# Performance work log

Measured on AMD Instinct MI355X. Metric: run time of the kernel, lower is better.

The kernel has to match this reference:

```python
import jax, jax.numpy as jnp
import numpy as np

B, S, D, L = 64, 512, 256, 3
NUM_BUCKETS = 1500  # RelativePositionBias default


def _ln(x, g, b):
    m = x.mean(-1, keepdims=True)
    v = x.var(-1, keepdims=True)
    return (x - m) * jax.lax.rsqrt(v + 1e-5) * g + b


def setup_inputs() -> dict:
    key = jax.random.key(0)
    ks = jax.random.split(key, 10)
    s = 0.02
    f32 = jnp.float32
    return dict(
        x=jax.random.normal(ks[0], (B, S, D), f32),
        mask=jnp.ones((B, S), jnp.int32),
        bias_table=jax.random.normal(ks[1], (NUM_BUCKETS,), f32) * s,  # n_heads=1
        ln_g=jnp.ones((L, D), f32), ln_b=jnp.zeros((L, D), f32),
        wq=jax.random.normal(ks[2], (L, D, D), f32) * s, bq=jnp.zeros((L, D), f32),
        wk=jax.random.normal(ks[3], (L, D, D), f32) * s, bk=jnp.zeros((L, D), f32),
        wv=jax.random.normal(ks[4], (L, D, D), f32) * s, bv=jnp.zeros((L, D), f32),
        wo=jax.random.normal(ks[5], (L, D, D), f32) * s, bo=jnp.zeros((L, D), f32),
        cm_ln_g=jnp.ones((L, D), f32), cm_ln_b=jnp.zeros((L, D), f32),
        w1=jax.random.normal(ks[6], (L, D, D), f32) * s, b1=jnp.zeros((L, D), f32),
        w2=jax.random.normal(ks[7], (L, D, D), f32) * s, b2=jnp.zeros((L, D), f32),
    )


def reference(x, mask, bias_table, ln_g, ln_b, wq, bq, wk, bk, wv, bv, wo, bo,
              cm_ln_g, cm_ln_b, w1, b1, w2, b2):
    slen = x.shape[1]
    # relative position bias (RelativePositionBias.compute_bias), n_heads=1
    pos = jnp.arange(slen)
    rel = pos[None, :] - pos[:, None]        # memory - context
    maxn = slen - 1                          # torch.max(rel)
    bucket = jnp.where(rel < 0, -rel + maxn, rel)
    cp = bias_table[bucket]                  # [S, S], broadcasts over batch
    scale = jnp.sqrt(jnp.asarray(x.shape[-1], x.dtype))  # sqrt(hid_dim // 1)
    pad = (mask == 0)[:, None, :]            # [B, 1, S] key-side padding mask
    neg = jnp.finfo(x.dtype).min
    for j in range(L):
        h = _ln(x, ln_g[j], ln_b[j])
        q = h @ wq[j] + bq[j]
        k = h @ wk[j] + bk[j]
        v = h @ wv[j] + bv[j]
        e = jnp.einsum('bqd,bkd->bqk', q, k) / scale + cp
        e = jnp.where(pad, neg, e)
        a = jax.nn.softmax(e, axis=-1)
        o = jnp.einsum('bqk,bkd->bqd', a, v) @ wo[j] + bo[j]
        x = h + _ln(o, ln_g[j], ln_b[j])     # same LayerNorm reused, per source
        c = _ln(x, cm_ln_g[j], cm_ln_b[j])
        x = x + (jax.nn.gelu(c @ w1[j] + b1[j], approximate=False) @ w2[j] + b2[j])
    return x
```

## Files before the change

kernel.cpp:

```cpp
#include <hip/hip_runtime.h>
#include <hip/hip_bf16.h>
#include <math.h>

#define D_HID 256
#define N_B   64
#define S_LEN 512
#define N_L   3
#define M_ROWS (N_B * S_LEN)

typedef __bf16 bf16_t;
typedef __bf16 bf16x8 __attribute__((ext_vector_type(8)));
typedef __bf16 bf16x4 __attribute__((ext_vector_type(4)));
typedef float  f32x4  __attribute__((ext_vector_type(4)));
typedef unsigned int u32;

__device__ __forceinline__ f32x4 mfma16(bf16x8 a, bf16x8 b, f32x4 c) {
    return __builtin_amdgcn_mfma_f32_16x16x32_bf16(a, b, c, 0, 0, 0);
}

__device__ __forceinline__ void gld_lds16(const void* g, void* l) {
    __builtin_amdgcn_global_load_lds((const __attribute__((address_space(1))) u32*)g,
                                     (__attribute__((address_space(3))) u32*)l, 16, 0, 0);
}

__device__ __forceinline__ u32 pk_bf16(float a, float b) {
    return (u32)(__hip_bfloat16_raw(__hip_bfloat16(a)).x) |
           ((u32)(__hip_bfloat16_raw(__hip_bfloat16(b)).x) << 16);
}

__global__ __launch_bounds__(256) void transpose_w(const float* __restrict__ w,
                                                   bf16_t* __restrict__ wt,
                                                   int layer_stride) {
    int i = blockIdx.x * 256 + threadIdx.x;
    int k = i & 255;
    int n = (i >> 8) & 255;
    int l = i >> 16;
    wt[(size_t)l * layer_stride + n * 256 + k] =
        (bf16_t)w[((size_t)l << 16) + ((size_t)k << 8) + n];
}

__global__ __launch_bounds__(256) void ln_fwd(const float* __restrict__ in,
                                              const float* __restrict__ g,
                                              const float* __restrict__ b,
                                              float* __restrict__ H,
                                              bf16_t* __restrict__ Hb) {
    int row  = blockIdx.x * 4 + (threadIdx.x >> 6);
    int lane = threadIdx.x & 63;
    float4 x = ((const float4*)(in + (size_t)row * D_HID))[lane];
    float s  = x.x + x.y + x.z + x.w;
    float sq = x.x * x.x + x.y * x.y + x.z * x.z + x.w * x.w;
#pragma unroll
    for (int o = 1; o < 64; o <<= 1) { s += __shfl_xor(s, o); sq += __shfl_xor(sq, o); }
    float mean = s * (1.f / D_HID);
    float rstd = rsqrtf(sq * (1.f / D_HID) - mean * mean + 1e-5f);
    float4 gv = ((const float4*)g)[lane];
    float4 bv = ((const float4*)b)[lane];
    float4 h;
    h.x = (x.x - mean) * rstd * gv.x + bv.x;
    h.y = (x.y - mean) * rstd * gv.y + bv.y;
    h.z = (x.z - mean) * rstd * gv.z + bv.z;
    h.w = (x.w - mean) * rstd * gv.w + bv.w;
    ((float4*)(H + (size_t)row * D_HID))[lane] = h;
    bf16x4 hb = { (bf16_t)h.x, (bf16_t)h.y, (bf16_t)h.z, (bf16_t)h.w };
    *((bf16x4*)(Hb + (size_t)row * D_HID) + lane) = hb;
}

__global__ __launch_bounds__(256) void ln_res_ln(const float* __restrict__ T,
                                                 const float* __restrict__ H,
                                                 const float* __restrict__ g,
                                                 const float* __restrict__ b,
                                                 const float* __restrict__ cg,
                                                 const float* __restrict__ cb,
                                                 float* __restrict__ X,
                                                 bf16_t* __restrict__ Cb) {
    int row  = blockIdx.x * 4 + (threadIdx.x >> 6);
    int lane = threadIdx.x & 63;
    float4 t = ((const float4*)(T + (size_t)row * D_HID))[lane];
    float s  = t.x + t.y + t.z + t.w;
    float sq = t.x * t.x + t.y * t.y + t.z * t.z + t.w * t.w;
#pragma unroll
    for (int o = 1; o < 64; o <<= 1) { s += __shfl_xor(s, o); sq += __shfl_xor(sq, o); }
    float mean = s * (1.f / D_HID);
    float rstd = rsqrtf(sq * (1.f / D_HID) - mean * mean + 1e-5f);
    float4 gv = ((const float4*)g)[lane];
    float4 bv = ((const float4*)b)[lane];
    float4 hh = ((const float4*)(H + (size_t)row * D_HID))[lane];
    float4 x;
    x.x = hh.x + (t.x - mean) * rstd * gv.x + bv.x;
    x.y = hh.y + (t.y - mean) * rstd * gv.y + bv.y;
    x.z = hh.z + (t.z - mean) * rstd * gv.z + bv.z;
    x.w = hh.w + (t.w - mean) * rstd * gv.w + bv.w;
    ((float4*)(X + (size_t)row * D_HID))[lane] = x;
    float s2  = x.x + x.y + x.z + x.w;
    float sq2 = x.x * x.x + x.y * x.y + x.z * x.z + x.w * x.w;
#pragma unroll
    for (int o = 1; o < 64; o <<= 1) { s2 += __shfl_xor(s2, o); sq2 += __shfl_xor(sq2, o); }
    float mean2 = s2 * (1.f / D_HID);
    float rstd2 = rsqrtf(sq2 * (1.f / D_HID) - mean2 * mean2 + 1e-5f);
    float4 cgv = ((const float4*)cg)[lane];
    float4 cbv = ((const float4*)cb)[lane];
    bf16x4 c = { (bf16_t)((x.x - mean2) * rstd2 * cgv.x + cbv.x),
                 (bf16_t)((x.y - mean2) * rstd2 * cgv.y + cbv.y),
                 (bf16_t)((x.z - mean2) * rstd2 * cgv.z + cbv.z),
                 (bf16_t)((x.w - mean2) * rstd2 * cgv.w + cbv.w) };
    *((bf16x4*)(Cb + (size_t)row * D_HID) + lane) = c;
}

__device__ __forceinline__ void gemm_core(const bf16_t* __restrict__ A,
                                          const bf16_t* __restrict__ W,
                                          int m0, int n0,
                                          bf16_t* As, bf16_t* Bs,
                                          f32x4 (&acc)[4][4]) {
    const int tid  = threadIdx.x;
    const int lane = tid & 63;
    const int wid  = tid >> 6;
    const int wm = wid >> 1, wn = wid & 1;
    const int r = lane & 15, g = lane >> 4;
#pragma unroll 1
    for (int kt = 0; kt < 4; ++kt) {
        if (kt) __syncthreads();
#pragma unroll
        for (int i = 0; i < 4; ++i) {
            const int base8 = i * 256 + wid * 64;
            const int idx8  = base8 + lane;
            const int row   = idx8 >> 3;
            const int sc8   = (idx8 & 7) ^ (row & 7);
            gld_lds16(A + (size_t)(m0 + row) * D_HID + kt * 64 + sc8 * 8, As + base8 * 8);
            gld_lds16(W + (size_t)(n0 + row) * D_HID + kt * 64 + sc8 * 8, Bs + base8 * 8);
        }
        __syncthreads();
#pragma unroll
        for (int ks = 0; ks < 2; ++ks) {
            bf16x8 af[4], bfr[4];
#pragma unroll
            for (int mt = 0; mt < 4; ++mt) {
                const int row = wm * 64 + mt * 16 + r;
                const int c8  = (ks * 4 + g) ^ (row & 7);
                af[mt] = *(const bf16x8*)(As + row * 64 + c8 * 8);
            }
#pragma unroll
            for (int nt = 0; nt < 4; ++nt) {
                const int row = wn * 64 + nt * 16 + r;
                const int c8  = (ks * 4 + g) ^ (row & 7);
                bfr[nt] = *(const bf16x8*)(Bs + row * 64 + c8 * 8);
            }
#pragma unroll
            for (int mt = 0; mt < 4; ++mt)
#pragma unroll
                for (int nt = 0; nt < 4; ++nt)
                    acc[mt][nt] = mfma16(af[mt], bfr[nt], acc[mt][nt]);
        }
    }
}

__global__ __launch_bounds__(256) void gemm_qkv(const bf16_t* __restrict__ A,
                                                const bf16_t* __restrict__ Wp,
                                                const float* __restrict__ bq,
                                                const float* __restrict__ bk,
                                                const float* __restrict__ bv,
                                                bf16_t* __restrict__ Qb,
                                                bf16_t* __restrict__ Kb,
                                                bf16_t* __restrict__ Vt) {
    __shared__ bf16_t As[128 * 64], Bs[128 * 64];
    f32x4 acc[4][4] = {};
    const int m0 = blockIdx.x * 128, n0 = blockIdx.y * 128;
    gemm_core(A, Wp, m0, n0, As, Bs, acc);
    const int lane = threadIdx.x & 63, wid = threadIdx.x >> 6;
    const int wm = wid >> 1, wn = wid & 1, r = lane & 15, g = lane >> 4;
#pragma unroll
    for (int nt = 0; nt < 4; ++nt) {
        const int col = n0 + wn * 64 + nt * 16 + r;
        const int t = col >> 8, cc = col & 255;
        const float bias = (t == 0 ? bq : t == 1 ? bk : bv)[cc];
#pragma unroll
        for (int mt = 0; mt < 4; ++mt)
#pragma unroll
            for (int rr = 0; rr < 4; ++rr) {
                const int row = m0 + wm * 64 + mt * 16 + g * 4 + rr;
                const float v = acc[mt][nt][rr] + bias;
                if (t == 0)      Qb[(size_t)row * D_HID + cc] = (bf16_t)v;
                else if (t == 1) Kb[(size_t)row * D_HID + cc] = (bf16_t)v;
                else             Vt[((size_t)(row >> 9) * D_HID + cc) * S_LEN + (row & 511)] = (bf16_t)v;
            }
    }
}

template <int EPI>
__global__ __launch_bounds__(256) void gemm_one(const bf16_t* __restrict__ A,
                                                const bf16_t* __restrict__ W,
                                                const float* __restrict__ bias,
                                                void* __restrict__ outp,
                                                const float* __restrict__ addsrc) {
    __shared__ bf16_t As[128 * 64], Bs[128 * 64];
    f32x4 acc[4][4] = {};
    const int m0 = blockIdx.x * 128, n0 = blockIdx.y * 128;
    gemm_core(A, W, m0, n0, As, Bs, acc);
    const int lane = threadIdx.x & 63, wid = threadIdx.x >> 6;
    const int wm = wid >> 1, wn = wid & 1, r = lane & 15, g = lane >> 4;
#pragma unroll
    for (int nt = 0; nt < 4; ++nt) {
        const int col = n0 + wn * 64 + nt * 16 + r;
        const float bv = bias[col];
#pragma unroll
        for (int mt = 0; mt < 4; ++mt)
#pragma unroll
            for (int rr = 0; rr < 4; ++rr) {
                const size_t idx = (size_t)(m0 + wm * 64 + mt * 16 + g * 4 + rr) * D_HID + col;
                float v = acc[mt][nt][rr] + bv;
                if constexpr (EPI == 1) {
                    v = 0.5f * v * (1.f + erff(v * 0.70710678118654752f));
                    ((bf16_t*)outp)[idx] = (bf16_t)v;
                } else if constexpr (EPI == 2) {
                    ((float*)outp)[idx] = v;
                } else {
                    ((float*)outp)[idx] = addsrc[idx] + v;
                }
            }
    }
}

__global__ __launch_bounds__(256) void attn_fwd(const bf16_t* __restrict__ Q,
                                                const bf16_t* __restrict__ K,
                                                const bf16_t* __restrict__ Vt,
                                                const float* __restrict__ btab,
                                                const int* __restrict__ mask,
                                                bf16_t* __restrict__ AO) {
    __shared__ float  bias_lds[1024];
    __shared__ float  mask_add[512];
    __shared__ bf16_t P_lds[32 * 64];
    __shared__ float  m_part[4][32], l_part[4][32];
    __shared__ bf16_t o_lds[32][264];

    const int tid = threadIdx.x, lane = tid & 63, w = tid >> 6;
    const int r = lane & 15, g = lane >> 4;

    const int lid = blockIdx.x;
    const int xcd = lid & 7, slot = lid >> 3;
    const int b  = xcd * 8 + (slot >> 4);
    const int q0 = (slot & 15) * 32;

    for (int i = tid; i < 1024; i += 256) {
        const int rel = i - 512;
        const int bucket = (rel < 0) ? (511 - rel) : rel;
        bias_lds[i] = btab[bucket];
    }
    for (int i = tid; i < 512; i += 256)
        mask_add[i] = mask[b * S_LEN + i] ? 0.f : -3.0e38f;
    __syncthreads();

    const bf16_t* Qp = Q  + ((size_t)b * S_LEN + q0) * D_HID;
    const bf16_t* Kp = K  + (size_t)b * S_LEN * D_HID;
    const bf16_t* Vp = Vt + (size_t)b * D_HID * S_LEN;

    f32x4 oacc[4][2] = {};
    float m_run[2] = {-3.0e38f, -3.0e38f};
    float l_run[2] = {0.f, 0.f};

#pragma unroll 1
    for (int kt = 0; kt < 8; ++kt) {
        const int k0 = kt * 64;
        f32x4 sacc[2] = {};
#pragma unroll
        for (int ks = 0; ks < 8; ++ks) {
            const int dk = ks * 32 + g * 8;
            bf16x8 kf  = *(const bf16x8*)(Kp + (size_t)(k0 + w * 16 + r) * D_HID + dk);
            bf16x8 qf0 = *(const bf16x8*)(Qp + (size_t)r * D_HID + dk);
            bf16x8 qf1 = *(const bf16x8*)(Qp + (size_t)(16 + r) * D_HID + dk);
            sacc[0] = mfma16(kf, qf0, sacc[0]);
            sacc[1] = mfma16(kf, qf1, sacc[1]);
        }
        float mx[2] = {-3.0e38f, -3.0e38f};
#pragma unroll
        for (int qb = 0; qb < 2; ++qb) {
            const int qg = q0 + qb * 16 + r;
#pragma unroll
            for (int rr = 0; rr < 4; ++rr) {
                const int kg = k0 + w * 16 + g * 4 + rr;
                float ev = sacc[qb][rr] * 0.0625f + bias_lds[kg - qg + 512] + mask_add[kg];
                sacc[qb][rr] = ev;
                mx[qb] = fmaxf(mx[qb], ev);
            }
            mx[qb] = fmaxf(mx[qb], __shfl_xor(mx[qb], 16));
            mx[qb] = fmaxf(mx[qb], __shfl_xor(mx[qb], 32));
        }
        if (g == 0) { m_part[w][r] = mx[0]; m_part[w][16 + r] = mx[1]; }
        __syncthreads();
        float mnew[2], fac[2];
#pragma unroll
        for (int qb = 0; qb < 2; ++qb) {
            const int q = qb * 16 + r;
            const float tm = fmaxf(fmaxf(m_part[0][q], m_part[1][q]),
                                   fmaxf(m_part[2][q], m_part[3][q]));
            mnew[qb] = fmaxf(m_run[qb], tm);
            fac[qb]  = __expf(m_run[qb] - mnew[qb]);
            m_run[qb] = mnew[qb];
        }
#pragma unroll
        for (int qb = 0; qb < 2; ++qb) {
            const float p0 = __expf(sacc[qb][0] - mnew[qb]);
            const float p1 = __expf(sacc[qb][1] - mnew[qb]);
            const float p2 = __expf(sacc[qb][2] - mnew[qb]);
            const float p3 = __expf(sacc[qb][3] - mnew[qb]);
            float ls = p0 + p1 + p2 + p3;
            ls += __shfl_xor(ls, 16);
            ls += __shfl_xor(ls, 32);
            if (g == 0) l_part[w][qb * 16 + r] = ls;
            const int q = qb * 16 + r;
            const int u = (2 * w + (g >> 1)) ^ (q & 7);
            uint2 pv; pv.x = pk_bf16(p0, p1); pv.y = pk_bf16(p2, p3);
            *(uint2*)((char*)P_lds + q * 128 + u * 16 + (g & 1) * 8) = pv;
        }
        __syncthreads();
#pragma unroll
        for (int qb = 0; qb < 2; ++qb) {
            const int q = qb * 16 + r;
            const float lt = l_part[0][q] + l_part[1][q] + l_part[2][q] + l_part[3][q];
            l_run[qb] = l_run[qb] * fac[qb] + lt;
        }
#pragma unroll
        for (int nt = 0; nt < 4; ++nt)
#pragma unroll
            for (int qb = 0; qb < 2; ++qb)
#pragma unroll
                for (int rr = 0; rr < 4; ++rr)
                    oacc[nt][qb][rr] *= fac[qb];
#pragma unroll
        for (int ks = 0; ks < 2; ++ks) {
            bf16x8 pf[2];
#pragma unroll
            for (int qb = 0; qb < 2; ++qb) {
                const int q = qb * 16 + r;
                const int u = (ks * 4 + g) ^ (q & 7);
                pf[qb] = *(const bf16x8*)((const char*)P_lds + q * 128 + u * 16);
            }
            __builtin_amdgcn_s_setprio(1);
#pragma unroll
            for (int nt = 0; nt < 4; ++nt) {
                bf16x8 vf = *(const bf16x8*)(Vp + (size_t)(w * 64 + nt * 16 + r) * S_LEN
                                                  + k0 + ks * 32 + g * 8);
                oacc[nt][0] = mfma16(vf, pf[0], oacc[nt][0]);
                oacc[nt][1] = mfma16(vf, pf[1], oacc[nt][1]);
            }
            __builtin_amdgcn_s_setprio(0);
        }
    }
    const float inv_l[2] = { 1.f / fmaxf(l_run[0], 1e-30f),
                             1.f / fmaxf(l_run[1], 1e-30f) };
#pragma unroll
    for (int nt = 0; nt < 4; ++nt)
#pragma unroll
        for (int qb = 0; qb < 2; ++qb) {
            const int q = qb * 16 + r;
            const int d = w * 64 + nt * 16 + g * 4;
            bf16x4 ob = { (bf16_t)(oacc[nt][qb][0] * inv_l[qb]),
                          (bf16_t)(oacc[nt][qb][1] * inv_l[qb]),
                          (bf16_t)(oacc[nt][qb][2] * inv_l[qb]),
                          (bf16_t)(oacc[nt][qb][3] * inv_l[qb]) };
            *(bf16x4*)&o_lds[q][d] = ob;
        }
    __syncthreads();
    bf16_t* Op = AO + ((size_t)b * S_LEN + q0) * D_HID;
#pragma unroll
    for (int it = 0; it < 4; ++it) {
        const int idx = it * 256 + tid;
        const int row = idx >> 5, u = idx & 31;
        bf16x8 vv = *(const bf16x8*)&o_lds[row][u * 8];
        *(bf16x8*)(Op + (size_t)row * D_HID + u * 8) = vv;
    }
}

extern "C" void kernel_launch(void* const* d_in, const int* in_sizes, int n_in,
                              void* d_out, int out_size, void* d_ws, size_t ws_size,
                              hipStream_t stream) {
    const float* x_in = (const float*)d_in[0];
    const int*   mask = (const int*)d_in[1];
    const float* btab = (const float*)d_in[2];
    const float* ln_g = (const float*)d_in[3];
    const float* ln_b = (const float*)d_in[4];
    const float* wq = (const float*)d_in[5];
    const float* bq = (const float*)d_in[6];
    const float* wk = (const float*)d_in[7];
    const float* bk = (const float*)d_in[8];
    const float* wv = (const float*)d_in[9];
    const float* bv = (const float*)d_in[10];
    const float* wo = (const float*)d_in[11];
    const float* bo = (const float*)d_in[12];
    const float* cg = (const float*)d_in[13];
    const float* cb = (const float*)d_in[14];
    const float* w1 = (const float*)d_in[15];
    const float* b1 = (const float*)d_in[16];
    const float* w2 = (const float*)d_in[17];
    const float* b2 = (const float*)d_in[18];
    float* out = (float*)d_out;

    char* p = (char*)d_ws;
    const size_t F32SZ  = (size_t)M_ROWS * D_HID * sizeof(float);
    const size_t BF16SZ = (size_t)M_ROWS * D_HID * sizeof(bf16_t);
    float*  H  = (float*)p;  p += F32SZ;
    float*  X  = (float*)p;  p += F32SZ;
    bf16_t* Hb = (bf16_t*)p; p += BF16SZ;
    bf16_t* Qb = (bf16_t*)p; p += BF16SZ;
    bf16_t* Kb = (bf16_t*)p;
    float*  T  = (float*)Kb;
    bf16_t* T1b = Kb;
    p += BF16SZ;
    bf16_t* Vt = (bf16_t*)p; p += BF16SZ;
    bf16_t* Wqkv = (bf16_t*)p; p += (size_t)N_L * 768 * 256 * sizeof(bf16_t);
    bf16_t* Wrest = (bf16_t*)p;
    bf16_t* AO = Hb;
    bf16_t* Cb = Qb;

    const int WELEMS = N_L * D_HID * D_HID;
    transpose_w<<<dim3(WELEMS / 256), dim3(256), 0, stream>>>(wq, Wqkv + 0 * 65536, 3 * 65536);
    transpose_w<<<dim3(WELEMS / 256), dim3(256), 0, stream>>>(wk, Wqkv + 1 * 65536, 3 * 65536);
    transpose_w<<<dim3(WELEMS / 256), dim3(256), 0, stream>>>(wv, Wqkv + 2 * 65536, 3 * 65536);
    transpose_w<<<dim3(WELEMS / 256), dim3(256), 0, stream>>>(wo, Wrest + (size_t)0 * WELEMS, 65536);
    transpose_w<<<dim3(WELEMS / 256), dim3(256), 0, stream>>>(w1, Wrest + (size_t)1 * WELEMS, 65536);
    transpose_w<<<dim3(WELEMS / 256), dim3(256), 0, stream>>>(w2, Wrest + (size_t)2 * WELEMS, 65536);

    const dim3 gblk(256, 1, 1);
    const dim3 grid_qkv(M_ROWS / 128, 6, 1);
    const dim3 grid_one(M_ROWS / 128, 2, 1);

    for (int j = 0; j < N_L; ++j) {
        const bf16_t* WQKVj = Wqkv + (size_t)j * 3 * 65536;
        const bf16_t* WOt = Wrest + ((size_t)0 * N_L + j) * 65536;
        const bf16_t* W1t = Wrest + ((size_t)1 * N_L + j) * 65536;
        const bf16_t* W2t = Wrest + ((size_t)2 * N_L + j) * 65536;

        ln_fwd<<<dim3(M_ROWS / 4), gblk, 0, stream>>>(j == 0 ? x_in : X,
                                                      ln_g + j * D_HID, ln_b + j * D_HID, H, Hb);
        gemm_qkv<<<grid_qkv, gblk, 0, stream>>>(Hb, WQKVj, bq + j * D_HID, bk + j * D_HID,
                                                bv + j * D_HID, Qb, Kb, Vt);
        attn_fwd<<<dim3(N_B * 16, 1, 1), gblk, 0, stream>>>(Qb, Kb, Vt, btab, mask, AO);
        gemm_one<2><<<grid_one, gblk, 0, stream>>>(AO, WOt, bo + j * D_HID, T, nullptr);
        ln_res_ln<<<dim3(M_ROWS / 4), gblk, 0, stream>>>(T, H, ln_g + j * D_HID, ln_b + j * D_HID,
                                                         cg + j * D_HID, cb + j * D_HID, X, Cb);
        gemm_one<1><<<grid_one, gblk, 0, stream>>>(Cb, W1t, b1 + j * D_HID, T1b, nullptr);
        gemm_one<3><<<grid_one, gblk, 0, stream>>>(T1b, W2t, b2 + j * D_HID,
                                                   (j == N_L - 1) ? (void*)out : (void*)X, X);
    }
}
```

Before: 715.8 us.

## Double-buffer GEMM LDS tiles, hoist Q and V loads in attention, fuse transposes

The GEMM core now double-buffers its A/B tiles in LDS, so the next K-tile is fetched while MFMAs run on the current one, and the number of barriers drops. In attention, Q fragments are loaded once into registers and V fragments are prefetched at the start of each key tile, and launch bounds request two blocks per CU. The six weight-transpose launches are merged into one. The cost is twice the GEMM LDS footprint and more registers in attention, which may lower occupancy.

```diff
diff --git a/kernel.cpp b/kernel.cpp
--- a/kernel.cpp
+++ b/kernel.cpp
@@ -28,15 +28,24 @@
            ((u32)(__hip_bfloat16_raw(__hip_bfloat16(b)).x) << 16);
 }
 
-__global__ __launch_bounds__(256) void transpose_w(const float* __restrict__ w,
-                                                   bf16_t* __restrict__ wt,
-                                                   int layer_stride) {
-    int i = blockIdx.x * 256 + threadIdx.x;
-    int k = i & 255;
-    int n = (i >> 8) & 255;
-    int l = i >> 16;
-    wt[(size_t)l * layer_stride + n * 256 + k] =
-        (bf16_t)w[((size_t)l << 16) + ((size_t)k << 8) + n];
+__global__ __launch_bounds__(256) void transpose_all(const float* __restrict__ wq,
+                                                     const float* __restrict__ wk,
+                                                     const float* __restrict__ wv,
+                                                     const float* __restrict__ wo,
+                                                     const float* __restrict__ w1,
+                                                     const float* __restrict__ w2,
+                                                     bf16_t* __restrict__ Wqkv,
+                                                     bf16_t* __restrict__ Wrest) {
+    const int t = blockIdx.y;
+    const float* src = t == 0 ? wq : t == 1 ? wk : t == 2 ? wv
+                     : t == 3 ? wo : t == 4 ? w1 : w2;
+    const int i = blockIdx.x * 256 + threadIdx.x;
+    const int k = i & 255;
+    const int n = (i >> 8) & 255;
+    const int l = i >> 16;
+    const bf16_t v = (bf16_t)src[((size_t)l << 16) + ((size_t)k << 8) + n];
+    if (t < 3) Wqkv[(size_t)l * 3 * 65536 + t * 65536 + n * 256 + k] = v;
+    else       Wrest[(size_t)(t - 3) * 196608 + l * 65536 + n * 256 + k] = v;
 }
 
 __global__ __launch_bounds__(256) void ln_fwd(const float* __restrict__ in,
@@ -106,49 +115,68 @@
     *((bf16x4*)(Cb + (size_t)row * D_HID) + lane) = c;
 }
 
+__device__ __forceinline__ void stage_tile(const bf16_t* __restrict__ A,
+                                           const bf16_t* __restrict__ W,
+                                           int m0, int n0, int kt,
+                                           bf16_t* As, bf16_t* Bs) {
+    const int lane = threadIdx.x & 63;
+    const int wid  = threadIdx.x >> 6;
+#pragma unroll
+    for (int i = 0; i < 4; ++i) {
+        const int base8 = i * 256 + wid * 64;
+        const int idx8  = base8 + lane;
+        const int row   = idx8 >> 3;
+        const int sc8   = (idx8 & 7) ^ (row & 7);
+        gld_lds16(A + (size_t)(m0 + row) * D_HID + kt * 64 + sc8 * 8, As + base8 * 8);
+        gld_lds16(W + (size_t)(n0 + row) * D_HID + kt * 64 + sc8 * 8, Bs + base8 * 8);
+    }
+}
+
+__device__ __forceinline__ void compute_tile(const bf16_t* As, const bf16_t* Bs,
+                                             f32x4 (&acc)[4][4]) {
+    const int lane = threadIdx.x & 63;
+    const int wid  = threadIdx.x >> 6;
+    const int wm = wid >> 1, wn = wid & 1;
+    const int r = lane & 15, g = lane >> 4;
+#pragma unroll
+    for (int ks = 0; ks < 2; ++ks) {
+        bf16x8 af[4], bfr[4];
+#pragma unroll
+        for (int mt = 0; mt < 4; ++mt) {
+            const int row = wm * 64 + mt * 16 + r;
+            const int c8  = (ks * 4 + g) ^ (row & 7);
+            af[mt] = *(const bf16x8*)(As + row * 64 + c8 * 8);
+        }
+#pragma unroll
+        for (int nt = 0; nt < 4; ++nt) {
+            const int row = wn * 64 + nt * 16 + r;
+            const int c8  = (ks * 4 + g) ^ (row & 7);
+            bfr[nt] = *(const bf16x8*)(Bs + row * 64 + c8 * 8);
+        }
+#pragma unroll
+        for (int mt = 0; mt < 4; ++mt)
+#pragma unroll
+            for (int nt = 0; nt < 4; ++nt)
+                acc[mt][nt] = mfma16(af[mt], bfr[nt], acc[mt][nt]);
+    }
+}
+
 __device__ __forceinline__ void gemm_core(const bf16_t* __restrict__ A,
                                           const bf16_t* __restrict__ W,
                                           int m0, int n0,
-                                          bf16_t* As, bf16_t* Bs,
+                                          bf16_t (&As)[2][8192], bf16_t (&Bs)[2][8192],
                                           f32x4 (&acc)[4][4]) {
-    const int tid  = threadIdx.x;
-    const int lane = tid & 63;
-    const int wid  = tid >> 6;
-    const int wm = wid >> 1, wn = wid & 1;
-    const int r = lane & 15, g = lane >> 4;
-#pragma unroll 1
+    stage_tile(A, W, m0, n0, 0, As[0], Bs[0]);
+    asm volatile("s_waitcnt vmcnt(0)" ::: "memory");
+    __builtin_amdgcn_s_barrier();
+#pragma unroll
     for (int kt = 0; kt < 4; ++kt) {
-        if (kt) __syncthreads();
-#pragma unroll
-        for (int i = 0; i < 4; ++i) {
-            const int base8 = i * 256 + wid * 64;
-            const int idx8  = base8 + lane;
-            const int row   = idx8 >> 3;
-            const int sc8   = (idx8 & 7) ^ (row & 7);
-            gld_lds16(A + (size_t)(m0 + row) * D_HID + kt * 64 + sc8 * 8, As + base8 * 8);
-            gld_lds16(W + (size_t)(n0 + row) * D_HID + kt * 64 + sc8 * 8, Bs + base8 * 8);
-        }
-        __syncthreads();
-#pragma unroll
-        for (int ks = 0; ks < 2; ++ks) {
-            bf16x8 af[4], bfr[4];
-#pragma unroll
-            for (int mt = 0; mt < 4; ++mt) {
-                const int row = wm * 64 + mt * 16 + r;
-                const int c8  = (ks * 4 + g) ^ (row & 7);
-                af[mt] = *(const bf16x8*)(As + row * 64 + c8 * 8);
-            }
-#pragma unroll
-            for (int nt = 0; nt < 4; ++nt) {
-                const int row = wn * 64 + nt * 16 + r;
-                const int c8  = (ks * 4 + g) ^ (row & 7);
-                bfr[nt] = *(const bf16x8*)(Bs + row * 64 + c8 * 8);
-            }
-#pragma unroll
-            for (int mt = 0; mt < 4; ++mt)
-#pragma unroll
-                for (int nt = 0; nt < 4; ++nt)
-                    acc[mt][nt] = mfma16(af[mt], bfr[nt], acc[mt][nt]);
+        const int cur = kt & 1;
+        if (kt < 3) stage_tile(A, W, m0, n0, kt + 1, As[cur ^ 1], Bs[cur ^ 1]);
+        compute_tile(As[cur], Bs[cur], acc);
+        if (kt < 3) {
+            asm volatile("s_waitcnt vmcnt(0)" ::: "memory");
+            __builtin_amdgcn_s_barrier();
         }
     }
 }
@@ -161,7 +189,7 @@
                                                 bf16_t* __restrict__ Qb,
                                                 bf16_t* __restrict__ Kb,
                                                 bf16_t* __restrict__ Vt) {
-    __shared__ bf16_t As[128 * 64], Bs[128 * 64];
+    __shared__ bf16_t As[2][8192], Bs[2][8192];
     f32x4 acc[4][4] = {};
     const int m0 = blockIdx.x * 128, n0 = blockIdx.y * 128;
     gemm_core(A, Wp, m0, n0, As, Bs, acc);
@@ -191,7 +219,7 @@
                                                 const float* __restrict__ bias,
                                                 void* __restrict__ outp,
                                                 const float* __restrict__ addsrc) {
-    __shared__ bf16_t As[128 * 64], Bs[128 * 64];
+    __shared__ bf16_t As[2][8192], Bs[2][8192];
     f32x4 acc[4][4] = {};
     const int m0 = blockIdx.x * 128, n0 = blockIdx.y * 128;
     gemm_core(A, W, m0, n0, As, Bs, acc);
@@ -219,12 +247,12 @@
     }
 }
 
-__global__ __launch_bounds__(256) void attn_fwd(const bf16_t* __restrict__ Q,
-                                                const bf16_t* __restrict__ K,
-                                                const bf16_t* __restrict__ Vt,
-                                                const float* __restrict__ btab,
-                                                const int* __restrict__ mask,
-                                                bf16_t* __restrict__ AO) {
+__global__ __launch_bounds__(256, 2) void attn_fwd(const bf16_t* __restrict__ Q,
+                                                   const bf16_t* __restrict__ K,
+                                                   const bf16_t* __restrict__ Vt,
+                                                   const float* __restrict__ btab,
+                                                   const int* __restrict__ mask,
+                                                   bf16_t* __restrict__ AO) {
     __shared__ float  bias_lds[1024];
     __shared__ float  mask_add[512];
     __shared__ bf16_t P_lds[32 * 64];
@@ -252,6 +280,13 @@
     const bf16_t* Kp = K  + (size_t)b * S_LEN * D_HID;
     const bf16_t* Vp = Vt + (size_t)b * D_HID * S_LEN;
 
+    bf16x8 qf[2][8];
+#pragma unroll
+    for (int ks = 0; ks < 8; ++ks) {
+        qf[0][ks] = *(const bf16x8*)(Qp + (size_t)r * D_HID + ks * 32 + g * 8);
+        qf[1][ks] = *(const bf16x8*)(Qp + (size_t)(16 + r) * D_HID + ks * 32 + g * 8);
+    }
+
     f32x4 oacc[4][2] = {};
     float m_run[2] = {-3.0e38f, -3.0e38f};
     float l_run[2] = {0.f, 0.f};
@@ -259,15 +294,20 @@
 #pragma unroll 1
     for (int kt = 0; kt < 8; ++kt) {
         const int k0 = kt * 64;
+        bf16x8 vpre[2][4];
+#pragma unroll
+        for (int ks = 0; ks < 2; ++ks)
+#pragma unroll
+            for (int nt = 0; nt < 4; ++nt)
+                vpre[ks][nt] = *(const bf16x8*)(Vp + (size_t)(w * 64 + nt * 16 + r) * S_LEN
+                                                     + k0 + ks * 32 + g * 8);
         f32x4 sacc[2] = {};
 #pragma unroll
         for (int ks = 0; ks < 8; ++ks) {
             const int dk = ks * 32 + g * 8;
-            bf16x8 kf  = *(const bf16x8*)(Kp + (size_t)(k0 + w * 16 + r) * D_HID + dk);
-            bf16x8 qf0 = *(const bf16x8*)(Qp + (size_t)r * D_HID + dk);
-            bf16x8 qf1 = *(const bf16x8*)(Qp + (size_t)(16 + r) * D_HID + dk);
-            sacc[0] = mfma16(kf, qf0, sacc[0]);
-            sacc[1] = mfma16(kf, qf1, sacc[1]);
+            bf16x8 kf = *(const bf16x8*)(Kp + (size_t)(k0 + w * 16 + r) * D_HID + dk);
+            sacc[0] = mfma16(kf, qf[0][ks], sacc[0]);
+            sacc[1] = mfma16(kf, qf[1][ks], sacc[1]);
         }
         float mx[2] = {-3.0e38f, -3.0e38f};
 #pragma unroll
@@ -336,10 +376,8 @@
             __builtin_amdgcn_s_setprio(1);
 #pragma unroll
             for (int nt = 0; nt < 4; ++nt) {
-                bf16x8 vf = *(const bf16x8*)(Vp + (size_t)(w * 64 + nt * 16 + r) * S_LEN
-                                                  + k0 + ks * 32 + g * 8);
-                oacc[nt][0] = mfma16(vf, pf[0], oacc[nt][0]);
-                oacc[nt][1] = mfma16(vf, pf[1], oacc[nt][1]);
+                oacc[nt][0] = mfma16(vpre[ks][nt], pf[0], oacc[nt][0]);
+                oacc[nt][1] = mfma16(vpre[ks][nt], pf[1], oacc[nt][1]);
             }
             __builtin_amdgcn_s_setprio(0);
         }
@@ -410,13 +448,7 @@
     bf16_t* AO = Hb;
     bf16_t* Cb = Qb;
 
-    const int WELEMS = N_L * D_HID * D_HID;
-    transpose_w<<<dim3(WELEMS / 256), dim3(256), 0, stream>>>(wq, Wqkv + 0 * 65536, 3 * 65536);
-    transpose_w<<<dim3(WELEMS / 256), dim3(256), 0, stream>>>(wk, Wqkv + 1 * 65536, 3 * 65536);
-    transpose_w<<<dim3(WELEMS / 256), dim3(256), 0, stream>>>(wv, Wqkv + 2 * 65536, 3 * 65536);
-    transpose_w<<<dim3(WELEMS / 256), dim3(256), 0, stream>>>(wo, Wrest + (size_t)0 * WELEMS, 65536);
-    transpose_w<<<dim3(WELEMS / 256), dim3(256), 0, stream>>>(w1, Wrest + (size_t)1 * WELEMS, 65536);
-    transpose_w<<<dim3(WELEMS / 256), dim3(256), 0, stream>>>(w2, Wrest + (size_t)2 * WELEMS, 65536);
+    transpose_all<<<dim3(768, 6), dim3(256), 0, stream>>>(wq, wk, wv, wo, w1, w2, Wqkv, Wrest);
 
     const dim3 gblk(256, 1, 1);
     const dim3 grid_qkv(M_ROWS / 128, 6, 1);
```

After: 687.7 us. 1.04x faster.
